# Kernel optimization log

Hardware: AMD Instinct MI355X
Metric: run time of the kernel (lower is better)

The kernel has to match this reference:

```python
import jax, jax.numpy as jnp
import numpy as np

N_EMBD = 1024
EXPAND = 2
D_STATE = 16
D_CONV = 4
D_INNER = N_EMBD * EXPAND
DT_RANK = 1  # d_state//16 if >1 else 1, with d_state=16 -> 1


def setup_inputs() -> dict:
    key = jax.random.key(0)
    ks = jax.random.split(key, 8)
    s = 0.02
    x = jax.random.normal(ks[0], (4, 2048, N_EMBD), dtype=jnp.float32)
    in_proj_w = jax.random.normal(ks[1], (N_EMBD, 2 * D_INNER), dtype=jnp.float32) * s
    conv_w = jax.random.normal(ks[2], (D_INNER, 1, D_CONV), dtype=jnp.float32) * s  # depthwise (O,I/g,K)
    conv_b = jax.random.normal(ks[3], (D_INNER,), dtype=jnp.float32) * s
    x_proj_w = jax.random.normal(ks[4], (D_INNER, DT_RANK + 2 * D_STATE), dtype=jnp.float32) * s
    dt_proj_w = jax.random.normal(ks[5], (DT_RANK, D_INNER), dtype=jnp.float32) * s
    dt_proj_b = jax.random.normal(ks[6], (D_INNER,), dtype=jnp.float32) * s
    A_log = jnp.tile(jnp.log(jnp.arange(1, D_STATE + 1, dtype=jnp.float32)), (D_INNER, 1))
    D = jnp.ones((D_INNER,), dtype=jnp.float32)
    out_proj_w = jax.random.normal(ks[7], (D_INNER, N_EMBD), dtype=jnp.float32) * s
    return {"x": x, "in_proj_w": in_proj_w, "conv_w": conv_w, "conv_b": conv_b,
            "x_proj_w": x_proj_w, "dt_proj_w": dt_proj_w, "dt_proj_b": dt_proj_b,
            "A_log": A_log, "D": D, "out_proj_w": out_proj_w}


def _mamba_forward(x, in_proj_w, conv_w, conv_b, x_proj_w, dt_proj_w, dt_proj_b, A_log, D, out_proj_w):
    Bsz, L, _ = x.shape
    d_inner = D.shape[0]
    n_state = A_log.shape[1]
    d_conv = conv_w.shape[-1]
    dt_rank = x_proj_w.shape[1] - 2 * n_state

    xr = x @ in_proj_w                      # [B,L,2*d_inner]
    x_ssm, res = jnp.split(xr, 2, axis=-1)  # each [B,L,d_inner]

    # depthwise causal conv: torch pads both sides by d_conv-1 then truncates to L,
    # equivalent to left-pad d_conv-1 only
    xc = x_ssm.transpose(0, 2, 1)           # [B,d_inner,L]
    xc = jax.lax.conv_general_dilated(
        xc, conv_w, window_strides=(1,), padding=[(d_conv - 1, 0)],
        dimension_numbers=("NCH", "OIH", "NCH"), feature_group_count=d_inner)
    xc = xc + conv_b[None, :, None]
    x_ssm = jax.nn.silu(xc.transpose(0, 2, 1))  # [B,L,d_inner]

    x_dbl = x_ssm @ x_proj_w                 # [B,L,dt_rank+2*n]
    dlt = x_dbl[..., :dt_rank]
    Bv = x_dbl[..., dt_rank:dt_rank + n_state]
    Cv = x_dbl[..., dt_rank + n_state:]
    delta = jax.nn.softplus(dlt @ dt_proj_w + dt_proj_b)  # [B,L,d_inner]

    A = -jnp.exp(A_log)                      # [d_inner,n]

    # time-major for scan
    xt = x_ssm.transpose(1, 0, 2)            # [L,B,d_inner]
    dtm = delta.transpose(1, 0, 2)           # [L,B,d_inner]
    Btm = Bv.transpose(1, 0, 2)              # [L,B,n]
    Ctm = Cv.transpose(1, 0, 2)              # [L,B,n]

    def step(h, inp):
        xt_, dt_, bt_, ct_ = inp
        A_bar = jnp.exp(dt_[..., None] * A)                         # [B,d_inner,n]
        h = A_bar * h + (bt_[:, None, :] * dt_[..., None]) * xt_[..., None]
        y = jnp.einsum("bdn,bn->bd", h, ct_) + D * xt_
        return h, y

    h0 = jnp.zeros((Bsz, d_inner, n_state), dtype=x.dtype)
    _, ys = jax.lax.scan(step, h0, (xt, dtm, Btm, Ctm))  # ys [L,B,d_inner]
    y = ys.transpose(1, 0, 2)                            # [B,L,d_inner]

    out = (y * jax.nn.silu(res)) @ out_proj_w            # [B,L,n_embd]
    return out


def reference(x, in_proj_w, conv_w, conv_b, x_proj_w, dt_proj_w, dt_proj_b, A_log, D, out_proj_w):
    return _mamba_forward(x, in_proj_w, conv_w, conv_b, x_proj_w, dt_proj_w, dt_proj_b, A_log, D, out_proj_w)
```

## Files before the change

### kernel.cpp

```cpp
#include <hip/hip_runtime.h>
#include <hip/hip_bf16.h>
#include <math.h>

#define SEQLEN 2048
#define NROWS  8192
#define DIN    2048
#define CHUNK  64
#define GCH    32

typedef __attribute__((ext_vector_type(8))) short short8;
typedef __attribute__((ext_vector_type(4))) float floatx4;

__device__ __forceinline__ float silu_f(float z) { return z / (1.f + __expf(-z)); }
__device__ __forceinline__ float bfbits2f(unsigned short u) {
  return __uint_as_float(((unsigned int)u) << 16);
}

__device__ __forceinline__ void gld_lds16(const void* gptr, void* lptr) {
  __builtin_amdgcn_global_load_lds((__attribute__((address_space(1))) unsigned int*)gptr,
                                   (__attribute__((address_space(3))) unsigned int*)lptr,
                                   16, 0, 0);
}

template <int BM>
__global__ __launch_bounds__(512) void gemm256(const __hip_bfloat16* __restrict__ A,
                                               const __hip_bfloat16* __restrict__ Bt,
                                               float* __restrict__ C,
                                               __hip_bfloat16* __restrict__ Cb,
                                               __hip_bfloat16* __restrict__ Gb,
                                               int N, int K) {
  constexpr int ABUF   = BM * 32;
  constexpr int ABYTES = ABUF * 2;
  constexpr int FM     = BM / 32;
  __shared__ unsigned short As[4 * ABUF];
  __shared__ unsigned short Bs[4 * 8192];
  const int tid  = threadIdx.x;
  const int lane = tid & 63;
  const int quad = lane >> 4;
  const int l15  = lane & 15;
  const int wv   = tid >> 6;
  const int wm   = wv >> 2;
  const int wn   = wv & 3;
  const int row0 = blockIdx.y * BM;
  const int col0 = blockIdx.x * 256;
  const int NT   = K >> 5;

  const int c0 = tid, c1 = 512 + tid;
  const int r0s = c0 >> 2, j0 = (c0 & 3) ^ ((r0s >> 1) & 3);
  const int r1s = c1 >> 2, j1 = (c1 & 3) ^ ((r1s >> 1) & 3);
  const __hip_bfloat16* a0p = A + (size_t)(row0 + r0s) * K + j0 * 8;
  const __hip_bfloat16* a1p = A + (size_t)(row0 + r1s) * K + j1 * 8;
  const __hip_bfloat16* b0p = Bt + (size_t)(col0 + r0s) * K + j0 * 8;
  const __hip_bfloat16* b1p = Bt + (size_t)(col0 + r1s) * K + j1 * 8;
  const int ldst0 = (wv * 64) * 16;
  const int ldst1 = (512 + wv * 64) * 16;

  const int swz   = (quad ^ ((l15 >> 1) & 3)) << 3;
  const int abase = (wm * (BM / 2) + l15) * 32 + swz;
  const int bbase = (wn * 64 + l15) * 32 + swz;

  floatx4 acc[FM][4] = {};

  if constexpr (BM == 256) {
    gld_lds16(a0p,      (char*)As + ldst0);
    gld_lds16(a1p,      (char*)As + ldst1);
    gld_lds16(b0p,      (char*)Bs + ldst0);
    gld_lds16(b1p,      (char*)Bs + ldst1);
    gld_lds16(a0p + 32, (char*)As + ABYTES + ldst0);
    gld_lds16(a1p + 32, (char*)As + ABYTES + ldst1);
    gld_lds16(b0p + 32, (char*)Bs + 16384 + ldst0);
    gld_lds16(b1p + 32, (char*)Bs + 16384 + ldst1);
    asm volatile("s_waitcnt vmcnt(4)" ::: "memory");
  } else {
    gld_lds16(a0p,      (char*)As + ldst0);
    gld_lds16(b0p,      (char*)Bs + ldst0);
    gld_lds16(b1p,      (char*)Bs + ldst1);
    gld_lds16(a0p + 32, (char*)As + ABYTES + ldst0);
    gld_lds16(b0p + 32, (char*)Bs + 16384 + ldst0);
    gld_lds16(b1p + 32, (char*)Bs + 16384 + ldst1);
    asm volatile("s_waitcnt vmcnt(3)" ::: "memory");
  }
  __builtin_amdgcn_s_barrier();
  __builtin_amdgcn_sched_barrier(0);

  for (int t = 0; t < NT; t++) {
    const unsigned short* Ab = As + (t & 3) * ABUF;
    const unsigned short* Bb = Bs + (t & 3) * 8192;
    const int t2     = t + 2;
    const int kof2   = t2 * 32;
    const int dbufA2 = (t2 & 3) * ABYTES;
    const int dbufB2 = (t2 & 3) * 16384;

    if constexpr (BM == 256) {
      short8 a[4], b[4];

#pragma unroll
      for (int m = 0; m < 4; m++) a[m] = *(const short8*)&Ab[abase + m * 512];
#pragma unroll
      for (int n = 0; n < 4; n++) b[n] = *(const short8*)&Bb[bbase + n * 512];
      if (t2 < NT) {
        gld_lds16(a0p + kof2, (char*)As + dbufA2 + ldst0);
        gld_lds16(a1p + kof2, (char*)As + dbufA2 + ldst1);
      }
      __builtin_amdgcn_s_barrier();
      asm volatile("s_waitcnt lgkmcnt(0)" ::: "memory");
      __builtin_amdgcn_sched_barrier(0);
      __builtin_amdgcn_s_setprio(1);
#pragma unroll
      for (int m = 0; m < 4; m++)
#pragma unroll
        for (int n = 0; n < 4; n++)
          acc[m][n] = __builtin_amdgcn_mfma_f32_16x16x32_bf16(a[m], b[n], acc[m][n], 0, 0, 0);
      __builtin_amdgcn_s_setprio(0);
      __builtin_amdgcn_sched_barrier(0);
      __builtin_amdgcn_s_barrier();

#pragma unroll
      for (int m = 0; m < 4; m++) a[m] = *(const short8*)&Ab[abase + (4 + m) * 512];
      if (t2 < NT) {
        gld_lds16(b0p + kof2, (char*)Bs + dbufB2 + ldst0);
        gld_lds16(b1p + kof2, (char*)Bs + dbufB2 + ldst1);
      }
      __builtin_amdgcn_s_barrier();
      asm volatile("s_waitcnt lgkmcnt(0)" ::: "memory");
      __builtin_amdgcn_sched_barrier(0);
      __builtin_amdgcn_s_setprio(1);
#pragma unroll
      for (int m = 0; m < 4; m++)
#pragma unroll
        for (int n = 0; n < 4; n++)
          acc[4 + m][n] = __builtin_amdgcn_mfma_f32_16x16x32_bf16(a[m], b[n], acc[4 + m][n], 0, 0, 0);
      __builtin_amdgcn_s_setprio(0);
      __builtin_amdgcn_sched_barrier(0);

      if (t < NT - 1) {
        if (t >= NT - 2) asm volatile("s_waitcnt vmcnt(0)" ::: "memory");
        else             asm volatile("s_waitcnt vmcnt(4)" ::: "memory");
        __builtin_amdgcn_s_barrier();
        __builtin_amdgcn_sched_barrier(0);
      }
    } else {
      short8 a[4], b[4];
#pragma unroll
      for (int m = 0; m < 4; m++) a[m] = *(const short8*)&Ab[abase + m * 512];
#pragma unroll
      for (int n = 0; n < 4; n++) b[n] = *(const short8*)&Bb[bbase + n * 512];
      if (t2 < NT) {
        gld_lds16(a0p + kof2, (char*)As + dbufA2 + ldst0);
        gld_lds16(b0p + kof2, (char*)Bs + dbufB2 + ldst0);
        gld_lds16(b1p + kof2, (char*)Bs + dbufB2 + ldst1);
      }
      __builtin_amdgcn_s_barrier();
      asm volatile("s_waitcnt lgkmcnt(0)" ::: "memory");
      __builtin_amdgcn_sched_barrier(0);
      __builtin_amdgcn_s_setprio(1);
#pragma unroll
      for (int m = 0; m < 4; m++)
#pragma unroll
        for (int n = 0; n < 4; n++)
          acc[m][n] = __builtin_amdgcn_mfma_f32_16x16x32_bf16(a[m], b[n], acc[m][n], 0, 0, 0);
      __builtin_amdgcn_s_setprio(0);
      __builtin_amdgcn_sched_barrier(0);

      if (t < NT - 1) {
        if (t >= NT - 2) asm volatile("s_waitcnt vmcnt(0)" ::: "memory");
        else             asm volatile("s_waitcnt vmcnt(3)" ::: "memory");
        __builtin_amdgcn_s_barrier();
        __builtin_amdgcn_sched_barrier(0);
      }
    }
  }

  const int Nh = N >> 1;
#pragma unroll
  for (int fm = 0; fm < FM; fm++) {
    int rbase = row0 + wm * (BM / 2) + fm * 16 + quad * 4;
#pragma unroll
    for (int n = 0; n < 4; n++) {
      int col = col0 + wn * 64 + n * 16 + l15;
#pragma unroll
      for (int r = 0; r < 4; r++) {
        float v = acc[fm][n][r];
        if (Cb) {
          if (col < Nh) Cb[(size_t)(rbase + r) * Nh + col] = __float2bfloat16(v);
          else          Gb[(size_t)(rbase + r) * Nh + col - Nh] = __float2bfloat16(silu_f(v));
        } else {
          C[(size_t)(rbase + r) * N + col] = v;
        }
      }
    }
  }
}

__global__ __launch_bounds__(256) void gemm_bf16(const __hip_bfloat16* __restrict__ A,
                                                 const __hip_bfloat16* __restrict__ Bt,
                                                 float* __restrict__ C,
                                                 int M, int N, int K) {
  __shared__ unsigned short As[128 * 64];
  __shared__ unsigned short Bs[128 * 64];
  const int tid  = threadIdx.x;
  const int lane = tid & 63;
  const int quad = lane >> 4;
  const int l15  = lane & 15;
  const int wv   = tid >> 6;
  const int wm   = wv >> 1;
  const int wn   = wv & 1;
  const int row0 = blockIdx.y * 128;
  const int col0 = blockIdx.x * 128;
  const int swz  = l15 & 7;

  floatx4 acc[4][4] = {};

  for (int k0 = 0; k0 < K; k0 += 64) {
#pragma unroll
    for (int i = 0; i < 4; i++) {
      int c = tid + i * 256;
      int r = c >> 3, j = c & 7;
      int js = j ^ (r & 7);
      gld_lds16(A + (size_t)(row0 + r) * K + k0 + js * 8,
                (char*)As + (size_t)(i * 256 + wv * 64) * 16);
      gld_lds16(Bt + (size_t)(col0 + r) * K + k0 + js * 8,
                (char*)Bs + (size_t)(i * 256 + wv * 64) * 16);
    }
    __syncthreads();
#pragma unroll
    for (int ks = 0; ks < 64; ks += 32) {
      const int sj = (((ks >> 3) + quad) ^ swz) << 3;
      short8 a[4], b[4];
#pragma unroll
      for (int t = 0; t < 4; t++) {
        a[t] = *(const short8*)&As[(wm * 64 + t * 16 + l15) * 64 + sj];
        b[t] = *(const short8*)&Bs[(wn * 64 + t * 16 + l15) * 64 + sj];
      }
#pragma unroll
      for (int tm = 0; tm < 4; tm++)
#pragma unroll
        for (int tn = 0; tn < 4; tn++)
          acc[tm][tn] = __builtin_amdgcn_mfma_f32_16x16x32_bf16(a[tm], b[tn], acc[tm][tn], 0, 0, 0);
    }
    __syncthreads();
  }
#pragma unroll
  for (int tm = 0; tm < 4; tm++) {
    int rbase = row0 + wm * 64 + tm * 16 + quad * 4;
#pragma unroll
    for (int tn = 0; tn < 4; tn++) {
      int col = col0 + wn * 64 + tn * 16 + l15;
#pragma unroll
      for (int r = 0; r < 4; r++)
        C[(size_t)(rbase + r) * N + col] = acc[tm][tn][r];
    }
  }
}

__global__ __launch_bounds__(256) void convert_bf16(const float* __restrict__ in,
                                                    __hip_bfloat16* __restrict__ out,
                                                    int n) {
  int i = (blockIdx.x * 256 + threadIdx.x) * 4;
  if (i >= n) return;
  float4 v = *reinterpret_cast<const float4*>(in + i);
  out[i + 0] = __float2bfloat16(v.x);
  out[i + 1] = __float2bfloat16(v.y);
  out[i + 2] = __float2bfloat16(v.z);
  out[i + 3] = __float2bfloat16(v.w);
}

__global__ __launch_bounds__(256) void transpose_bf16(const float* __restrict__ w,
                                                      __hip_bfloat16* __restrict__ wt,
                                                      int K, int N) {
  __shared__ float tile[32][33];
  int n0 = blockIdx.x * 32, k0 = blockIdx.y * 32;
  int tx = threadIdx.x;
#pragma unroll
  for (int i = threadIdx.y; i < 32; i += 8)
    tile[i][tx] = w[(size_t)(k0 + i) * N + n0 + tx];
  __syncthreads();
#pragma unroll
  for (int i = threadIdx.y; i < 32; i += 8)
    wt[(size_t)(n0 + i) * K + k0 + tx] = __float2bfloat16(tile[tx][i]);
}

__global__ __launch_bounds__(256) void pack_xproj(const float* __restrict__ w,
                                                  __hip_bfloat16* __restrict__ wtp) {
  int idx = blockIdx.x * 256 + threadIdx.x;
  int n = idx >> 11;
  int k = idx & 2047;
  int src = (n == 0) ? 0 : ((n >= 4 && n < 36) ? (n - 3) : -1);
  float v = (src >= 0) ? w[(size_t)k * 33 + src] : 0.f;
  wtp[idx] = __float2bfloat16(v);
}

__global__ __launch_bounds__(256) void conv_silu_kernel(const __hip_bfloat16* __restrict__ xssm,
                                                        const float* __restrict__ conv_w,
                                                        const float* __restrict__ conv_b,
                                                        float* __restrict__ x_c,
                                                        __hip_bfloat16* __restrict__ x_cb) {
  int idx = blockIdx.x * blockDim.x + threadIdx.x;
  if (idx >= NROWS * DIN) return;
  int d = idx & (DIN - 1);
  int row = idx >> 11;
  int l = row & (SEQLEN - 1);
  float acc = conv_b[d];
#pragma unroll
  for (int k = 0; k < 4; k++) {
    int ls = l + k - 3;
    if (ls >= 0)
      acc = fmaf(conv_w[d * 4 + k],
                 __bfloat162float(xssm[(size_t)(row + k - 3) * DIN + d]), acc);
  }
  float v = silu_f(acc);
  x_c[idx] = v;
  x_cb[idx] = __float2bfloat16(v);
}

__global__ __launch_bounds__(256) void scan_passA(const float* __restrict__ x_c,
                                                  const float* __restrict__ xd,
                                                  const float* __restrict__ dt_w,
                                                  const float* __restrict__ dt_b,
                                                  float* __restrict__ hend,
                                                  float* __restrict__ sumdelta) {
  const int d = blockIdx.x * 256 + threadIdx.x;
  const int b = blockIdx.y >> 5;
  const int g = blockIdx.y & 31;
  const int ch = b * DIN + d;
  const float dtw = dt_w[d], dtb = dt_b[d];
  float h[16];
#pragma unroll
  for (int n = 0; n < 16; n++) h[n] = 0.f;
  float sd = 0.f;
  const int row = b * SEQLEN + g * CHUNK;
  const float* xdr = xd + (size_t)row * 128;
  const float* xcr = x_c + (size_t)row * DIN + d;
  float dl = xdr[0];
  float4 B0 = *(const float4*)(xdr + 4);
  float4 B1 = *(const float4*)(xdr + 8);
  float4 B2 = *(const float4*)(xdr + 12);
  float4 B3 = *(const float4*)(xdr + 16);
  float xv = *xcr;
  for (int l = 0; l < CHUNK; l++) {
    const int adv = (l < CHUNK - 1) ? 1 : 0;
    const float* xdn = xdr + adv * 128;
    const float* xcn = xcr + adv * DIN;
    float dl_n = xdn[0];
    float4 B0n = *(const float4*)(xdn + 4);
    float4 B1n = *(const float4*)(xdn + 8);
    float4 B2n = *(const float4*)(xdn + 12);
    float4 B3n = *(const float4*)(xdn + 16);
    float xv_n = *xcn;

    float z = fmaf(dl, dtw, dtb);
    float e = __expf(z);
    float denom = 1.f + e;
    float delta = __logf(denom);
    float r = __builtin_amdgcn_rcpf(denom);
    sd += delta;
    float dx = delta * xv;
    float p2 = r * r, p3 = p2 * r, p4 = p2 * p2;
    float b2 = p4 * p4, b3 = b2 * p4;
    h[0]  = fmaf(r,       h[0],  B0.x * dx);
    h[1]  = fmaf(p2,      h[1],  B0.y * dx);
    h[2]  = fmaf(p3,      h[2],  B0.z * dx);
    h[3]  = fmaf(p4,      h[3],  B0.w * dx);
    h[4]  = fmaf(p4 * r,  h[4],  B1.x * dx);
    h[5]  = fmaf(p4 * p2, h[5],  B1.y * dx);
    h[6]  = fmaf(p4 * p3, h[6],  B1.z * dx);
    h[7]  = fmaf(b2,      h[7],  B1.w * dx);
    h[8]  = fmaf(b2 * r,  h[8],  B2.x * dx);
    h[9]  = fmaf(b2 * p2, h[9],  B2.y * dx);
    h[10] = fmaf(b2 * p3, h[10], B2.z * dx);
    h[11] = fmaf(b3,      h[11], B2.w * dx);
    h[12] = fmaf(b3 * r,  h[12], B3.x * dx);
    h[13] = fmaf(b3 * p2, h[13], B3.y * dx);
    h[14] = fmaf(b3 * p3, h[14], B3.z * dx);
    h[15] = fmaf(b3 * p4, h[15], B3.w * dx);

    dl = dl_n; xv = xv_n; B0 = B0n; B1 = B1n; B2 = B2n; B3 = B3n;
    xdr = xdn; xcr = xcn;
  }
  size_t base = ((size_t)g * 8192 + ch) * 16;
#pragma unroll
  for (int n = 0; n < 16; n += 4) {
    float4 hv = {h[n], h[n + 1], h[n + 2], h[n + 3]};
    *reinterpret_cast<float4*>(&hend[base + n]) = hv;
  }
  sumdelta[(size_t)g * 8192 + ch] = sd;
}

__global__ __launch_bounds__(256) void scan_passB(const float* __restrict__ A_log,
                                                  const float* __restrict__ sumdelta,
                                                  const float* __restrict__ hend,
                                                  float* __restrict__ hinit) {
  int t = blockIdx.x * 256 + threadIdx.x;
  int ch = t >> 2, q = t & 3;
  int d = ch & (DIN - 1);
  float4 al = *reinterpret_cast<const float4*>(&A_log[d * 16 + q * 4]);
  const float An0 = -__expf(al.x), An1 = -__expf(al.y),
              An2 = -__expf(al.z), An3 = -__expf(al.w);
  float4 h = {0.f, 0.f, 0.f, 0.f};
#pragma unroll
  for (int g = 0; g < GCH; g++) {
    size_t base = ((size_t)g * 8192 + ch) * 16 + q * 4;
    *reinterpret_cast<float4*>(&hinit[base]) = h;
    float sd = sumdelta[(size_t)g * 8192 + ch];
    float4 he = *reinterpret_cast<const float4*>(&hend[base]);
    h.x = fmaf(__expf(An0 * sd), h.x, he.x);
    h.y = fmaf(__expf(An1 * sd), h.y, he.y);
    h.z = fmaf(__expf(An2 * sd), h.z, he.z);
    h.w = fmaf(__expf(An3 * sd), h.w, he.w);
  }
}

__global__ __launch_bounds__(256) void scan_passC(const float* __restrict__ x_c,
                                                  const float* __restrict__ xd,
                                                  const float* __restrict__ dt_w,
                                                  const float* __restrict__ dt_b,
                                                  const float* __restrict__ Dp,
                                                  const float* __restrict__ hinit,
                                                  const __hip_bfloat16* __restrict__ gate,
                                                  __hip_bfloat16* __restrict__ outg) {
  const int d = blockIdx.x * 256 + threadIdx.x;
  const int b = blockIdx.y >> 5;
  const int g = blockIdx.y & 31;
  const int ch = b * DIN + d;
  const float dtw = dt_w[d], dtb = dt_b[d], Dd = Dp[d];
  float h[16];
  {
    size_t base = ((size_t)g * 8192 + ch) * 16;
#pragma unroll
    for (int n = 0; n < 16; n += 4) {
      float4 hv = *reinterpret_cast<const float4*>(&hinit[base + n]);
      h[n] = hv.x; h[n + 1] = hv.y; h[n + 2] = hv.z; h[n + 3] = hv.w;
    }
  }
  const int row0 = b * SEQLEN + g * CHUNK;
  const float* xdr = xd + (size_t)row0 * 128;
  const float* xcr = x_c + (size_t)row0 * DIN + d;
  const __hip_bfloat16* gtr = gate + (size_t)row0 * DIN + d;
  __hip_bfloat16* otr = outg + (size_t)row0 * DIN + d;
  float dl = xdr[0];
  float4 B0 = *(const float4*)(xdr + 4);
  float4 B1 = *(const float4*)(xdr + 8);
  float4 B2 = *(const float4*)(xdr + 12);
  float4 B3 = *(const float4*)(xdr + 16);
  float4 C0 = *(const float4*)(xdr + 20);
  float4 C1 = *(const float4*)(xdr + 24);
  float4 C2 = *(const float4*)(xdr + 28);
  float4 C3 = *(const float4*)(xdr + 32);
  float xv = *xcr;
  float gv = bfbits2f(*(const unsigned short*)gtr);
  for (int l = 0; l < CHUNK; l++) {
    const int adv = (l < CHUNK - 1) ? 1 : 0;
    const float* xdn = xdr + adv * 128;
    const float* xcn = xcr + adv * DIN;
    const __hip_bfloat16* gtn = gtr + adv * DIN;
    float dl_n = xdn[0];
    float4 B0n = *(const float4*)(xdn + 4);
    float4 B1n = *(const float4*)(xdn + 8);
    float4 B2n = *(const float4*)(xdn + 12);
    float4 B3n = *(const float4*)(xdn + 16);
    float4 C0n = *(const float4*)(xdn + 20);
    float4 C1n = *(const float4*)(xdn + 24);
    float4 C2n = *(const float4*)(xdn + 28);
    float4 C3n = *(const float4*)(xdn + 32);
    float xv_n = *xcn;
    float gv_n = bfbits2f(*(const unsigned short*)gtn);

    float z = fmaf(dl, dtw, dtb);
    float e = __expf(z);
    float denom = 1.f + e;
    float delta = __logf(denom);
    float r = __builtin_amdgcn_rcpf(denom);
    float dx = delta * xv;
    float p2 = r * r, p3 = p2 * r, p4 = p2 * p2;
    float b2 = p4 * p4, b3 = b2 * p4;
    h[0]  = fmaf(r,       h[0],  B0.x * dx);
    h[1]  = fmaf(p2,      h[1],  B0.y * dx);
    h[2]  = fmaf(p3,      h[2],  B0.z * dx);
    h[3]  = fmaf(p4,      h[3],  B0.w * dx);
    h[4]  = fmaf(p4 * r,  h[4],  B1.x * dx);
    h[5]  = fmaf(p4 * p2, h[5],  B1.y * dx);
    h[6]  = fmaf(p4 * p3, h[6],  B1.z * dx);
    h[7]  = fmaf(b2,      h[7],  B1.w * dx);
    h[8]  = fmaf(b2 * r,  h[8],  B2.x * dx);
    h[9]  = fmaf(b2 * p2, h[9],  B2.y * dx);
    h[10] = fmaf(b2 * p3, h[10], B2.z * dx);
    h[11] = fmaf(b3,      h[11], B2.w * dx);
    h[12] = fmaf(b3 * r,  h[12], B3.x * dx);
    h[13] = fmaf(b3 * p2, h[13], B3.y * dx);
    h[14] = fmaf(b3 * p3, h[14], B3.z * dx);
    h[15] = fmaf(b3 * p4, h[15], B3.w * dx);

    float y0 = fmaf(h[0],  C0.x, fmaf(h[1],  C0.y, fmaf(h[2],  C0.z, h[3]  * C0.w)));
    float y1 = fmaf(h[4],  C1.x, fmaf(h[5],  C1.y, fmaf(h[6],  C1.z, h[7]  * C1.w)));
    float y2 = fmaf(h[8],  C2.x, fmaf(h[9],  C2.y, fmaf(h[10], C2.z, h[11] * C2.w)));
    float y3 = fmaf(h[12], C3.x, fmaf(h[13], C3.y, fmaf(h[14], C3.z, h[15] * C3.w)));
    float y = (y0 + y1) + (y2 + y3);
    *(unsigned short*)otr = __bfloat16_as_ushort(__float2bfloat16(fmaf(Dd, xv, y) * gv));

    dl = dl_n; xv = xv_n; gv = gv_n;
    B0 = B0n; B1 = B1n; B2 = B2n; B3 = B3n;
    C0 = C0n; C1 = C1n; C2 = C2n; C3 = C3n;
    xdr = xdn; xcr = xcn; gtr = gtn; otr += adv * DIN;
  }
}

extern "C" void kernel_launch(void* const* d_in, const int* in_sizes, int n_in,
                              void* d_out, int out_size, void* d_ws, size_t ws_size,
                              hipStream_t stream) {
  const float* x         = (const float*)d_in[0];
  const float* in_proj_w = (const float*)d_in[1];
  const float* conv_w    = (const float*)d_in[2];
  const float* conv_b    = (const float*)d_in[3];
  const float* x_proj_w  = (const float*)d_in[4];
  const float* dt_proj_w = (const float*)d_in[5];
  const float* dt_proj_b = (const float*)d_in[6];
  const float* A_log     = (const float*)d_in[7];
  const float* Dp        = (const float*)d_in[8];
  const float* out_proj_w= (const float*)d_in[9];
  float* out = (float*)d_out;

  const size_t MB = 1u << 20;
  char* ws = (char*)d_ws;
  __hip_bfloat16* xb      = (__hip_bfloat16*)(ws);
  float*          xdbl128 = (float*)(ws);
  float*          sumdl   = (float*)(ws + 4 * MB);
  __hip_bfloat16* wtp     = (__hip_bfloat16*)(ws + 5 * MB);
  __hip_bfloat16* wt3     = (__hip_bfloat16*)(ws + 6 * MB);
  __hip_bfloat16* wt1     = (__hip_bfloat16*)(ws + 16 * MB);
  __hip_bfloat16* xssm_bf = (__hip_bfloat16*)(ws + 24 * MB);
  float*          hend    = (float*)(ws + 24 * MB);
  __hip_bfloat16* gate_bf = (__hip_bfloat16*)(ws + 56 * MB);
  float*          x_c     = (float*)(ws + 88 * MB);
  __hip_bfloat16* x_cb    = (__hip_bfloat16*)(ws + 152 * MB);
  __hip_bfloat16* gated   = (__hip_bfloat16*)(ws + 152 * MB);
  float*          hinit   = (float*)(ws + 184 * MB);

  convert_bf16<<<(NROWS * 1024) / 1024, 256, 0, stream>>>(x, xb, NROWS * 1024);
  transpose_bf16<<<dim3(4096 / 32, 1024 / 32), dim3(32, 8), 0, stream>>>(in_proj_w, wt1, 1024, 4096);

  gemm256<256><<<dim3(4096 / 256, NROWS / 256), 512, 0, stream>>>(
      xb, wt1, (float*)nullptr, xssm_bf, gate_bf, 4096, 1024);

  conv_silu_kernel<<<(NROWS * DIN) / 256, 256, 0, stream>>>(xssm_bf, conv_w, conv_b, x_c, x_cb);

  pack_xproj<<<(128 * 2048) / 256, 256, 0, stream>>>(x_proj_w, wtp);
  gemm_bf16<<<dim3(1, NROWS / 128), 256, 0, stream>>>(
      x_cb, wtp, xdbl128, NROWS, 128, 2048);

  scan_passA<<<dim3(DIN / 256, 4 * GCH), 256, 0, stream>>>(x_c, xdbl128, dt_proj_w, dt_proj_b, hend, sumdl);
  scan_passB<<<128, 256, 0, stream>>>(A_log, sumdl, hend, hinit);
  scan_passC<<<dim3(DIN / 256, 4 * GCH), 256, 0, stream>>>(x_c, xdbl128, dt_proj_w, dt_proj_b, Dp, hinit,
                                                           gate_bf, gated);

  transpose_bf16<<<dim3(1024 / 32, 2048 / 32), dim3(32, 8), 0, stream>>>(out_proj_w, wt3, 2048, 1024);

  gemm256<128><<<dim3(1024 / 256, NROWS / 128), 512, 0, stream>>>(
      gated, wt3, out, (__hip_bfloat16*)nullptr, (__hip_bfloat16*)nullptr, 1024, 2048);
}
```

Measured before the change: 465.2 us.

## Deepen GEMM LDS prefetch to three stages and drop mid-iteration barriers

The bf16 MFMA GEMM now keeps three K-tiles in flight in its four-buffer LDS ring instead of two. The prologue issues three stages, and each iteration prefetches tile t+3 with the vmcnt thresholds adjusted to match. For the 256-row tile, all eight A fragments are read from LDS before compute, so A and B for the next stage are prefetched together and the two intra-iteration workgroup barriers are removed, leaving one barrier per K step. This aims to hide more global-load latency and reduce barrier stalls, at the cost of more live registers for the A fragments and tighter reliance on the ring-buffer reuse distance being correct.

```diff
diff --git a/kernel.cpp b/kernel.cpp
--- a/kernel.cpp
+++ b/kernel.cpp
@@ -61,49 +61,44 @@
 
   floatx4 acc[FM][4] = {};
 
-  if constexpr (BM == 256) {
-    gld_lds16(a0p,      (char*)As + ldst0);
-    gld_lds16(a1p,      (char*)As + ldst1);
-    gld_lds16(b0p,      (char*)Bs + ldst0);
-    gld_lds16(b1p,      (char*)Bs + ldst1);
-    gld_lds16(a0p + 32, (char*)As + ABYTES + ldst0);
-    gld_lds16(a1p + 32, (char*)As + ABYTES + ldst1);
-    gld_lds16(b0p + 32, (char*)Bs + 16384 + ldst0);
-    gld_lds16(b1p + 32, (char*)Bs + 16384 + ldst1);
-    asm volatile("s_waitcnt vmcnt(4)" ::: "memory");
-  } else {
-    gld_lds16(a0p,      (char*)As + ldst0);
-    gld_lds16(b0p,      (char*)Bs + ldst0);
-    gld_lds16(b1p,      (char*)Bs + ldst1);
-    gld_lds16(a0p + 32, (char*)As + ABYTES + ldst0);
-    gld_lds16(b0p + 32, (char*)Bs + 16384 + ldst0);
-    gld_lds16(b1p + 32, (char*)Bs + 16384 + ldst1);
-    asm volatile("s_waitcnt vmcnt(3)" ::: "memory");
-  }
+#pragma unroll
+  for (int p = 0; p < 3; p++) {
+    const int kof = p * 32;
+    const int dA = p * ABYTES, dB = p * 16384;
+    gld_lds16(a0p + kof, (char*)As + dA + ldst0);
+    if constexpr (BM == 256) gld_lds16(a1p + kof, (char*)As + dA + ldst1);
+    gld_lds16(b0p + kof, (char*)Bs + dB + ldst0);
+    gld_lds16(b1p + kof, (char*)Bs + dB + ldst1);
+  }
+  if constexpr (BM == 256) asm volatile("s_waitcnt vmcnt(8)" ::: "memory");
+  else                     asm volatile("s_waitcnt vmcnt(6)" ::: "memory");
   __builtin_amdgcn_s_barrier();
   __builtin_amdgcn_sched_barrier(0);
 
   for (int t = 0; t < NT; t++) {
     const unsigned short* Ab = As + (t & 3) * ABUF;
     const unsigned short* Bb = Bs + (t & 3) * 8192;
-    const int t2     = t + 2;
-    const int kof2   = t2 * 32;
-    const int dbufA2 = (t2 & 3) * ABYTES;
-    const int dbufB2 = (t2 & 3) * 16384;
+    const int t3     = t + 3;
+    const int kof3   = t3 * 32;
+    const int dbufA3 = (t3 & 3) * ABYTES;
+    const int dbufB3 = (t3 & 3) * 16384;
 
     if constexpr (BM == 256) {
-      short8 a[4], b[4];
-
+      short8 a[8], b[4];
 #pragma unroll
       for (int m = 0; m < 4; m++) a[m] = *(const short8*)&Ab[abase + m * 512];
 #pragma unroll
       for (int n = 0; n < 4; n++) b[n] = *(const short8*)&Bb[bbase + n * 512];
-      if (t2 < NT) {
-        gld_lds16(a0p + kof2, (char*)As + dbufA2 + ldst0);
-        gld_lds16(a1p + kof2, (char*)As + dbufA2 + ldst1);
+      __builtin_amdgcn_sched_barrier(0);
+      if (t3 < NT) {
+        gld_lds16(a0p + kof3, (char*)As + dbufA3 + ldst0);
+        gld_lds16(a1p + kof3, (char*)As + dbufA3 + ldst1);
+        gld_lds16(b0p + kof3, (char*)Bs + dbufB3 + ldst0);
+        gld_lds16(b1p + kof3, (char*)Bs + dbufB3 + ldst1);
       }
-      __builtin_amdgcn_s_barrier();
-      asm volatile("s_waitcnt lgkmcnt(0)" ::: "memory");
+#pragma unroll
+      for (int m = 4; m < 8; m++) a[m] = *(const short8*)&Ab[abase + m * 512];
+      asm volatile("s_waitcnt lgkmcnt(4)" ::: "memory");
       __builtin_amdgcn_sched_barrier(0);
       __builtin_amdgcn_s_setprio(1);
 #pragma unroll
@@ -113,29 +108,21 @@
           acc[m][n] = __builtin_amdgcn_mfma_f32_16x16x32_bf16(a[m], b[n], acc[m][n], 0, 0, 0);
       __builtin_amdgcn_s_setprio(0);
       __builtin_amdgcn_sched_barrier(0);
-      __builtin_amdgcn_s_barrier();
-
-#pragma unroll
-      for (int m = 0; m < 4; m++) a[m] = *(const short8*)&Ab[abase + (4 + m) * 512];
-      if (t2 < NT) {
-        gld_lds16(b0p + kof2, (char*)Bs + dbufB2 + ldst0);
-        gld_lds16(b1p + kof2, (char*)Bs + dbufB2 + ldst1);
-      }
-      __builtin_amdgcn_s_barrier();
       asm volatile("s_waitcnt lgkmcnt(0)" ::: "memory");
       __builtin_amdgcn_sched_barrier(0);
       __builtin_amdgcn_s_setprio(1);
 #pragma unroll
-      for (int m = 0; m < 4; m++)
+      for (int m = 4; m < 8; m++)
 #pragma unroll
         for (int n = 0; n < 4; n++)
-          acc[4 + m][n] = __builtin_amdgcn_mfma_f32_16x16x32_bf16(a[m], b[n], acc[4 + m][n], 0, 0, 0);
+          acc[m][n] = __builtin_amdgcn_mfma_f32_16x16x32_bf16(a[m], b[n], acc[m][n], 0, 0, 0);
       __builtin_amdgcn_s_setprio(0);
       __builtin_amdgcn_sched_barrier(0);
 
       if (t < NT - 1) {
-        if (t >= NT - 2) asm volatile("s_waitcnt vmcnt(0)" ::: "memory");
-        else             asm volatile("s_waitcnt vmcnt(4)" ::: "memory");
+        if (t < NT - 3)       asm volatile("s_waitcnt vmcnt(8)" ::: "memory");
+        else if (t == NT - 3) asm volatile("s_waitcnt vmcnt(4)" ::: "memory");
+        else                  asm volatile("s_waitcnt vmcnt(0)" ::: "memory");
         __builtin_amdgcn_s_barrier();
         __builtin_amdgcn_sched_barrier(0);
       }
@@ -145,12 +132,12 @@
       for (int m = 0; m < 4; m++) a[m] = *(const short8*)&Ab[abase + m * 512];
 #pragma unroll
       for (int n = 0; n < 4; n++) b[n] = *(const short8*)&Bb[bbase + n * 512];
-      if (t2 < NT) {
-        gld_lds16(a0p + kof2, (char*)As + dbufA2 + ldst0);
-        gld_lds16(b0p + kof2, (char*)Bs + dbufB2 + ldst0);
-        gld_lds16(b1p + kof2, (char*)Bs + dbufB2 + ldst1);
+      __builtin_amdgcn_sched_barrier(0);
+      if (t3 < NT) {
+        gld_lds16(a0p + kof3, (char*)As + dbufA3 + ldst0);
+        gld_lds16(b0p + kof3, (char*)Bs + dbufB3 + ldst0);
+        gld_lds16(b1p + kof3, (char*)Bs + dbufB3 + ldst1);
       }
-      __builtin_amdgcn_s_barrier();
       asm volatile("s_waitcnt lgkmcnt(0)" ::: "memory");
       __builtin_amdgcn_sched_barrier(0);
       __builtin_amdgcn_s_setprio(1);
@@ -163,8 +150,9 @@
       __builtin_amdgcn_sched_barrier(0);
 
       if (t < NT - 1) {
-        if (t >= NT - 2) asm volatile("s_waitcnt vmcnt(0)" ::: "memory");
-        else             asm volatile("s_waitcnt vmcnt(3)" ::: "memory");
+        if (t < NT - 3)       asm volatile("s_waitcnt vmcnt(6)" ::: "memory");
+        else if (t == NT - 3) asm volatile("s_waitcnt vmcnt(3)" ::: "memory");
+        else                  asm volatile("s_waitcnt vmcnt(0)" ::: "memory");
         __builtin_amdgcn_s_barrier();
         __builtin_amdgcn_sched_barrier(0);
       }
```

New measurement: 461.7 us. No clear change (-0.8%).
